# Kernel tuning notes

Hardware: AMD Instinct MI355X
Metric: run time of the kernel (lower is better)

## Reference

```python
import jax, jax.numpy as jnp
import numpy as np

N_MOD, DEPTH, DIM_E = 8, 2, 128   # n experts, routing depth, codebook dim
C, H, W, B = 128, 32, 32, 16      # channels, spatial, batch


def setup_inputs() -> dict:
    key = jax.random.key(0)
    ks = jax.random.split(key, 5)
    s = lambda fan: 1.0 / np.sqrt(fan)
    x = jax.random.normal(ks[0], (B, C, H, W), jnp.float32)
    # controller: 1x1 conv == linear on globally-pooled features
    W_ctl = jax.random.normal(ks[1], (DEPTH * DIM_E, C), jnp.float32) * s(C)
    b_ctl = jnp.zeros((DEPTH * DIM_E,), jnp.float32)
    # VQ codebook: [dim_embeddings, n_modules]
    emb = jax.random.normal(ks[2], (DIM_E, N_MOD), jnp.float32)
    # expert conv weights (shared across depth, as in the module list)
    W_exp = jax.random.normal(ks[3], (N_MOD, C, C, 3, 3), jnp.float32) * s(C * 9)
    b_exp = jnp.zeros((N_MOD, C), jnp.float32)
    return {"x": x, "W_ctl": W_ctl, "b_ctl": b_ctl, "emb": emb,
            "W_exp": W_exp, "b_exp": b_exp}


def reference(x, W_ctl, b_ctl, emb, W_exp, b_exp):
    Bn = x.shape[0]
    # controller: 1x1 conv then AdaptiveAvgPool2d(1) == pool then linear
    pooled = x.mean(axis=(2, 3))                      # [B, C]
    ctl = (pooled @ W_ctl.T + b_ctl).reshape(Bn, DIM_E, DEPTH)  # [B, D, depth]
    # nearest-embedding routing indices (argmin over codebook, no grad path)
    d2 = ((ctl[:, :, :, None] - emb[None, :, None, :]) ** 2).sum(axis=1)  # [B, depth, n_mod]
    idx = jnp.argmin(d2, axis=-1)                     # [B, depth]
    # quantized controller codes from detached ctl (same indices here)
    ctl_sg = jax.lax.stop_gradient(ctl)
    d2n = ((ctl_sg[:, :, :, None] - emb[None, :, None, :]) ** 2).sum(axis=1)
    idx_n = jnp.argmin(d2n, axis=-1)                  # [B, depth]
    ctl_nearest = jnp.transpose(emb[:, idx_n], (1, 0, 2))  # [B, D, depth]
    # dispatch: run all experts as one grouped conv, then gather per example
    Wflat = W_exp.reshape(N_MOD * C, C, 3, 3)
    y = x
    for t in range(DEPTH):
        out = jax.lax.conv_general_dilated(
            y, Wflat, window_strides=(1, 1), padding='SAME',
            dimension_numbers=('NCHW', 'OIHW', 'NCHW'))  # [B, n_mod*C, H, W]
        out = out.reshape(Bn, N_MOD, C, H, W) + b_exp[None, :, :, None, None]
        out = jax.nn.relu(out)
        y = out[jnp.arange(Bn), idx[:, t]]            # [B, C, H, W]
    return y, ctl, ctl_nearest
```

## Files before the change

kernel.cpp:

```cpp
#include <hip/hip_runtime.h>
#include <cstddef>

#define NMOD   8
#define DEPTH_ 2
#define DIME   128
#define CCH    128
#define HH     32
#define WW     32
#define BB     16
#define HWPX   (HH*WW)

#define CO_TILE 4
#define CI_TILE 4
#define CI_HALF 64
#define TROWS   34
#define TSTRIDE 36
#define PF_N    4

__global__ __launch_bounds__(256) void pool_kernel(
    const float* __restrict__ x, float* __restrict__ pooled)
{
    const int ch   = blockIdx.x * 4 + (threadIdx.x >> 6);
    const int lane = threadIdx.x & 63;
    const float* xc = x + (size_t)ch * HWPX;

    float4 s4 = {0.f, 0.f, 0.f, 0.f};
    #pragma unroll
    for (int k = 0; k < 4; ++k) {
        const float4 v = *(const float4*)(xc + (size_t)(lane + k * 64) * 4);
        s4.x += v.x; s4.y += v.y; s4.z += v.z; s4.w += v.w;
    }
    float s = (s4.x + s4.y) + (s4.z + s4.w);
    #pragma unroll
    for (int off = 32; off; off >>= 1) s += __shfl_xor(s, off, 64);
    if (lane == 0) pooled[ch] = s * (1.0f / HWPX);
}

__global__ __launch_bounds__(256) void ctl_kernel(
    const float* __restrict__ pooled, const float* __restrict__ W_ctl,
    const float* __restrict__ b_ctl, const float* __restrict__ emb,
    float* __restrict__ ctl_out, float* __restrict__ ctln_out,
    int* __restrict__ idx_out)
{
    const int b   = blockIdx.x;
    const int tid = threadIdx.x;

    __shared__ float pld[CCH];
    __shared__ float ctlrow[DIME * DEPTH_];
    __shared__ float d2s[DEPTH_ * NMOD];
    __shared__ int   sidx[DEPTH_];

    if (tid < CCH / 4)
        ((float4*)pld)[tid] = ((const float4*)(pooled + (size_t)b * CCH))[tid];
    __syncthreads();

    {
        const float4* wr = (const float4*)(W_ctl + (size_t)tid * CCH);
        const float4* pv = (const float4*)pld;
        float a0 = 0.f, a1 = 0.f, a2 = 0.f, a3 = 0.f;
        #pragma unroll
        for (int k = 0; k < 32; k += 4) {
            const float4 w0 = wr[k + 0], p0 = pv[k + 0];
            const float4 w1 = wr[k + 1], p1 = pv[k + 1];
            const float4 w2 = wr[k + 2], p2 = pv[k + 2];
            const float4 w3 = wr[k + 3], p3 = pv[k + 3];
            a0 = fmaf(w0.x, p0.x, fmaf(w0.y, p0.y, fmaf(w0.z, p0.z, fmaf(w0.w, p0.w, a0))));
            a1 = fmaf(w1.x, p1.x, fmaf(w1.y, p1.y, fmaf(w1.z, p1.z, fmaf(w1.w, p1.w, a1))));
            a2 = fmaf(w2.x, p2.x, fmaf(w2.y, p2.y, fmaf(w2.z, p2.z, fmaf(w2.w, p2.w, a2))));
            a3 = fmaf(w3.x, p3.x, fmaf(w3.y, p3.y, fmaf(w3.z, p3.z, fmaf(w3.w, p3.w, a3))));
        }
        const float s = b_ctl[tid] + ((a0 + a1) + (a2 + a3));
        ctlrow[tid] = s;
        ctl_out[(size_t)b * (DIME * DEPTH_) + tid] = s;
    }
    __syncthreads();

    {
        const int p = tid >> 4;
        const int sub = tid & 15;
        const int t = p >> 3, mm = p & 7;
        float s = 0.f;
        #pragma unroll
        for (int k = 0; k < 8; ++k) {
            const int e = sub * 8 + k;
            const float d = ctlrow[e * DEPTH_ + t] - emb[e * NMOD + mm];
            s = fmaf(d, d, s);
        }
        #pragma unroll
        for (int off = 8; off; off >>= 1) s += __shfl_xor(s, off, 16);
        if (sub == 0) d2s[p] = s;
    }
    __syncthreads();

    if (tid < DEPTH_) {
        float best = d2s[tid * NMOD];
        int bi = 0;
        for (int m = 1; m < NMOD; ++m) {
            const float d = d2s[tid * NMOD + m];
            if (d < best) { best = d; bi = m; }
        }
        sidx[tid] = bi;
        idx_out[b * DEPTH_ + tid] = bi;
    }
    __syncthreads();

    {
        const int e = tid >> 1, t = tid & 1;
        ctln_out[(size_t)b * (DIME * DEPTH_) + e * DEPTH_ + t] =
            emb[e * NMOD + sidx[t]];
    }
}

__global__ __launch_bounds__(256, 4) void conv_kernel(
    const float* __restrict__ in, const float* __restrict__ W_exp,
    const int* __restrict__ idx, int t,
    float* __restrict__ p0, float* __restrict__ p1)
{
    const int cog  = blockIdx.x;
    const int b    = blockIdx.y;
    const int half = blockIdx.z;
    const int tid  = threadIdx.x;
    const int ci_base = half * CI_HALF;
    const int m   = __builtin_amdgcn_readfirstlane(idx[b * DEPTH_ + t]);
    const int co0 = cog * CO_TILE;

    __shared__ float tile[CI_TILE * TROWS * TSTRIDE];

    const float* wb = W_exp + (size_t)m * CCH * (CCH * 9) + (size_t)ci_base * 9;
    const float* wc0 = wb + (size_t)(co0 + 0) * (CCH * 9);
    const float* wc1 = wb + (size_t)(co0 + 1) * (CCH * 9);
    const float* wc2 = wb + (size_t)(co0 + 2) * (CCH * 9);
    const float* wc3 = wb + (size_t)(co0 + 3) * (CCH * 9);

    for (int i = tid; i < CI_TILE * TROWS * TSTRIDE; i += 256) tile[i] = 0.f;

    const int h  = tid >> 3;
    const int w4 = (tid & 7) * 4;

    float acc[4][CO_TILE];
    #pragma unroll
    for (int p = 0; p < 4; ++p)
        #pragma unroll
        for (int c = 0; c < CO_TILE; ++c) acc[p][c] = 0.f;

    const float* ing = in + (size_t)b * CCH * HWPX + (size_t)ci_base * HWPX;

    float4 pf[PF_N];
    #pragma unroll
    for (int k = 0; k < PF_N; ++k)
        pf[k] = *(const float4*)(ing + (size_t)(tid + k * 256) * 4);

    __syncthreads();

    for (int ci0 = 0; ci0 < CI_HALF; ci0 += CI_TILE) {
        #pragma unroll
        for (int k = 0; k < PF_N; ++k) {
            const int q   = tid + k * 256;
            const int cil = q >> 8;
            const int p4  = q & 255;
            const int hh  = p4 >> 3;
            const int ww  = (p4 & 7) * 4;
            float* dst = &tile[cil * (TROWS * TSTRIDE) + (hh + 1) * TSTRIDE + (ww + 1)];
            dst[0] = pf[k].x; dst[1] = pf[k].y; dst[2] = pf[k].z; dst[3] = pf[k].w;
        }
        if (ci0 + CI_TILE < CI_HALF) {
            const float* src = ing + (size_t)(ci0 + CI_TILE) * HWPX;
            #pragma unroll
            for (int k = 0; k < PF_N; ++k)
                pf[k] = *(const float4*)(src + (size_t)(tid + k * 256) * 4);
        }
        __syncthreads();

        #pragma unroll
        for (int cil = 0; cil < CI_TILE; ++cil) {
            const float* trow = &tile[cil * (TROWS * TSTRIDE)];
            const int    cw   = (ci0 + cil) * 9;

            float wr[CO_TILE][9];
            #pragma unroll
            for (int j = 0; j < 9; ++j) {
                wr[0][j] = wc0[cw + j];
                wr[1][j] = wc1[cw + j];
                wr[2][j] = wc2[cw + j];
                wr[3][j] = wc3[cw + j];
            }

            #pragma unroll
            for (int kh = 0; kh < 3; ++kh) {
                const float* r = trow + (h + kh) * TSTRIDE + w4;
                const float4 a4 = *(const float4*)(r);
                const float2 a2 = *(const float2*)(r + 4);
                const float in6[6] = {a4.x, a4.y, a4.z, a4.w, a2.x, a2.y};
                #pragma unroll
                for (int kw = 0; kw < 3; ++kw) {
                    #pragma unroll
                    for (int p = 0; p < 4; ++p) {
                        const float v = in6[p + kw];
                        acc[p][0] = fmaf(v, wr[0][kh * 3 + kw], acc[p][0]);
                        acc[p][1] = fmaf(v, wr[1][kh * 3 + kw], acc[p][1]);
                        acc[p][2] = fmaf(v, wr[2][kh * 3 + kw], acc[p][2]);
                        acc[p][3] = fmaf(v, wr[3][kh * 3 + kw], acc[p][3]);
                    }
                }
            }
        }
        __syncthreads();
    }

    float* outp = (half == 0) ? p0 : p1;
    float* ob = outp + ((size_t)b * CCH + co0) * HWPX + h * WW + w4;
    #pragma unroll
    for (int c = 0; c < CO_TILE; ++c) {
        float4 v;
        v.x = acc[0][c]; v.y = acc[1][c]; v.z = acc[2][c]; v.w = acc[3][c];
        *(float4*)(ob + (size_t)c * HWPX) = v;
    }
}

__global__ __launch_bounds__(256) void combine_kernel(
    const float* __restrict__ p0, const float* __restrict__ p1,
    const float* __restrict__ b_exp, const int* __restrict__ idx, int t,
    float* __restrict__ outp)
{
    const int i4 = blockIdx.x * 256 + threadIdx.x;
    const int b  = i4 >> 15;
    const int co = (i4 >> 8) & (CCH - 1);
    const int m  = idx[b * DEPTH_ + t];
    const float bv = b_exp[m * CCH + co];
    const float4 a = ((const float4*)p0)[i4];
    const float4 c = ((const float4*)p1)[i4];
    float4 v;
    v.x = fmaxf(a.x + c.x + bv, 0.f);
    v.y = fmaxf(a.y + c.y + bv, 0.f);
    v.z = fmaxf(a.z + c.z + bv, 0.f);
    v.w = fmaxf(a.w + c.w + bv, 0.f);
    ((float4*)outp)[i4] = v;
}

extern "C" void kernel_launch(void* const* d_in, const int* in_sizes, int n_in,
                              void* d_out, int out_size, void* d_ws, size_t ws_size,
                              hipStream_t stream) {
    const float* x     = (const float*)d_in[0];
    const float* W_ctl = (const float*)d_in[1];
    const float* b_ctl = (const float*)d_in[2];
    const float* emb   = (const float*)d_in[3];
    const float* W_exp = (const float*)d_in[4];
    const float* b_exp = (const float*)d_in[5];

    float* out      = (float*)d_out;
    float* y_out    = out;
    float* ctl_out  = out + (size_t)BB * CCH * HWPX;
    float* ctln_out = ctl_out + BB * DIME * DEPTH_;

    float* wsA    = (float*)d_ws;
    int*   idxp   = (int*)((char*)d_ws + (size_t)BB * CCH * HWPX * sizeof(float));
    float* pooled = (float*)((char*)idxp + 128);
    float* xbuf   = (float*)d_in[0];

    const int NY4 = (BB * CCH * HWPX) / 4;

    pool_kernel<<<(BB * CCH) / 4, 256, 0, stream>>>(x, pooled);
    ctl_kernel<<<BB, 256, 0, stream>>>(pooled, W_ctl, b_ctl, emb,
                                       ctl_out, ctln_out, idxp);

    conv_kernel<<<dim3(CCH / CO_TILE, BB, 2), 256, 0, stream>>>(
        x, W_exp, idxp, 0, y_out, wsA);
    combine_kernel<<<NY4 / 256, 256, 0, stream>>>(
        y_out, wsA, b_exp, idxp, 0, wsA);

    conv_kernel<<<dim3(CCH / CO_TILE, BB, 2), 256, 0, stream>>>(
        wsA, W_exp, idxp, 1, y_out, xbuf);
    combine_kernel<<<NY4 / 256, 256, 0, stream>>>(
        y_out, xbuf, b_exp, idxp, 1, y_out);
}
```

Measured before the change: 220.6 us.

## Replace LDS-tiled conv input staging with direct global loads and zero-page halo

The conv kernel no longer stages input channels through a shared-memory tile with barriers. Each thread now loads its own 3x3 halo (a float4 plus left and right neighbours for three rows) straight from global memory, one channel ahead in registers. Out-of-bounds positions point at a small zeroed page that the pool kernel writes, with a zero stride. This removes LDS writes and the __syncthreads per channel group, but makes every thread issue many small overlapping global loads that rely on L1/L2 for reuse.

```diff
diff --git a/kernel.cpp b/kernel.cpp
--- a/kernel.cpp
+++ b/kernel.cpp
@@ -11,15 +11,14 @@
 #define HWPX   (HH*WW)
 
 #define CO_TILE 4
-#define CI_TILE 4
 #define CI_HALF 64
-#define TROWS   34
-#define TSTRIDE 36
-#define PF_N    4
 
 __global__ __launch_bounds__(256) void pool_kernel(
-    const float* __restrict__ x, float* __restrict__ pooled)
-{
+    const float* __restrict__ x, float* __restrict__ pooled,
+    float* __restrict__ zpage)
+{
+    if (blockIdx.x == 0 && threadIdx.x < 64) zpage[threadIdx.x] = 0.f;
+
     const int ch   = blockIdx.x * 4 + (threadIdx.x >> 6);
     const int lane = threadIdx.x & 63;
     const float* xc = x + (size_t)ch * HWPX;
@@ -113,7 +112,7 @@
 
 __global__ __launch_bounds__(256, 4) void conv_kernel(
     const float* __restrict__ in, const float* __restrict__ W_exp,
-    const int* __restrict__ idx, int t,
+    const int* __restrict__ idx, int t, const float* __restrict__ zpage,
     float* __restrict__ p0, float* __restrict__ p1)
 {
     const int cog  = blockIdx.x;
@@ -124,18 +123,30 @@
     const int m   = __builtin_amdgcn_readfirstlane(idx[b * DEPTH_ + t]);
     const int co0 = cog * CO_TILE;
 
-    __shared__ float tile[CI_TILE * TROWS * TSTRIDE];
-
     const float* wb = W_exp + (size_t)m * CCH * (CCH * 9) + (size_t)ci_base * 9;
     const float* wc0 = wb + (size_t)(co0 + 0) * (CCH * 9);
     const float* wc1 = wb + (size_t)(co0 + 1) * (CCH * 9);
     const float* wc2 = wb + (size_t)(co0 + 2) * (CCH * 9);
     const float* wc3 = wb + (size_t)(co0 + 3) * (CCH * 9);
 
-    for (int i = tid; i < CI_TILE * TROWS * TSTRIDE; i += 256) tile[i] = 0.f;
-
     const int h  = tid >> 3;
-    const int w4 = (tid & 7) * 4;
+    const int wp = tid & 7;
+    const int w4 = wp * 4;
+
+    const float* xb = in + (size_t)b * CCH * HWPX + (size_t)ci_base * HWPX;
+    const float* pm[3]; const float* pl[3]; const float* pr[3];
+    int sm[3], sl[3], sr[3];
+    #pragma unroll
+    for (int kh = 0; kh < 3; ++kh) {
+        const int row = h + kh - 1;
+        const bool vr = (unsigned)row < 32u;
+        const float* rbase = xb + row * WW;
+        const bool vl = vr && (wp > 0);
+        const bool vR = vr && (wp < 7);
+        pm[kh] = vr ? (rbase + w4)     : zpage;  sm[kh] = vr ? HWPX : 0;
+        pl[kh] = vl ? (rbase + w4 - 1) : zpage;  sl[kh] = vl ? HWPX : 0;
+        pr[kh] = vR ? (rbase + w4 + 4) : zpage;  sr[kh] = vR ? HWPX : 0;
+    }
 
     float acc[4][CO_TILE];
     #pragma unroll
@@ -143,69 +154,58 @@
         #pragma unroll
         for (int c = 0; c < CO_TILE; ++c) acc[p][c] = 0.f;
 
-    const float* ing = in + (size_t)b * CCH * HWPX + (size_t)ci_base * HWPX;
-
-    float4 pf[PF_N];
-    #pragma unroll
-    for (int k = 0; k < PF_N; ++k)
-        pf[k] = *(const float4*)(ing + (size_t)(tid + k * 256) * 4);
-
-    __syncthreads();
-
-    for (int ci0 = 0; ci0 < CI_HALF; ci0 += CI_TILE) {
-        #pragma unroll
-        for (int k = 0; k < PF_N; ++k) {
-            const int q   = tid + k * 256;
-            const int cil = q >> 8;
-            const int p4  = q & 255;
-            const int hh  = p4 >> 3;
-            const int ww  = (p4 & 7) * 4;
-            float* dst = &tile[cil * (TROWS * TSTRIDE) + (hh + 1) * TSTRIDE + (ww + 1)];
-            dst[0] = pf[k].x; dst[1] = pf[k].y; dst[2] = pf[k].z; dst[3] = pf[k].w;
-        }
-        if (ci0 + CI_TILE < CI_HALF) {
-            const float* src = ing + (size_t)(ci0 + CI_TILE) * HWPX;
+    float4 cm[3]; float cl[3], cr[3];
+    #pragma unroll
+    for (int kh = 0; kh < 3; ++kh) {
+        cm[kh] = *(const float4*)pm[kh];
+        cl[kh] = *pl[kh];
+        cr[kh] = *pr[kh];
+    }
+
+    auto body = [&](int ci) {
+        const int cw = ci * 9;
+        float wr[CO_TILE][9];
+        #pragma unroll
+        for (int j = 0; j < 9; ++j) {
+            wr[0][j] = wc0[cw + j];
+            wr[1][j] = wc1[cw + j];
+            wr[2][j] = wc2[cw + j];
+            wr[3][j] = wc3[cw + j];
+        }
+        #pragma unroll
+        for (int kh = 0; kh < 3; ++kh) {
+            const float in6[6] = {cl[kh], cm[kh].x, cm[kh].y, cm[kh].z,
+                                  cm[kh].w, cr[kh]};
             #pragma unroll
-            for (int k = 0; k < PF_N; ++k)
-                pf[k] = *(const float4*)(src + (size_t)(tid + k * 256) * 4);
-        }
-        __syncthreads();
-
-        #pragma unroll
-        for (int cil = 0; cil < CI_TILE; ++cil) {
-            const float* trow = &tile[cil * (TROWS * TSTRIDE)];
-            const int    cw   = (ci0 + cil) * 9;
-
-            float wr[CO_TILE][9];
-            #pragma unroll
-            for (int j = 0; j < 9; ++j) {
-                wr[0][j] = wc0[cw + j];
-                wr[1][j] = wc1[cw + j];
-                wr[2][j] = wc2[cw + j];
-                wr[3][j] = wc3[cw + j];
-            }
-
-            #pragma unroll
-            for (int kh = 0; kh < 3; ++kh) {
-                const float* r = trow + (h + kh) * TSTRIDE + w4;
-                const float4 a4 = *(const float4*)(r);
-                const float2 a2 = *(const float2*)(r + 4);
-                const float in6[6] = {a4.x, a4.y, a4.z, a4.w, a2.x, a2.y};
+            for (int kw = 0; kw < 3; ++kw) {
                 #pragma unroll
-                for (int kw = 0; kw < 3; ++kw) {
-                    #pragma unroll
-                    for (int p = 0; p < 4; ++p) {
-                        const float v = in6[p + kw];
-                        acc[p][0] = fmaf(v, wr[0][kh * 3 + kw], acc[p][0]);
-                        acc[p][1] = fmaf(v, wr[1][kh * 3 + kw], acc[p][1]);
-                        acc[p][2] = fmaf(v, wr[2][kh * 3 + kw], acc[p][2]);
-                        acc[p][3] = fmaf(v, wr[3][kh * 3 + kw], acc[p][3]);
-                    }
+                for (int p = 0; p < 4; ++p) {
+                    const float v = in6[p + kw];
+                    acc[p][0] = fmaf(v, wr[0][kh * 3 + kw], acc[p][0]);
+                    acc[p][1] = fmaf(v, wr[1][kh * 3 + kw], acc[p][1]);
+                    acc[p][2] = fmaf(v, wr[2][kh * 3 + kw], acc[p][2]);
+                    acc[p][3] = fmaf(v, wr[3][kh * 3 + kw], acc[p][3]);
                 }
             }
         }
-        __syncthreads();
-    }
+    };
+
+    for (int ci = 0; ci < CI_HALF - 1; ++ci) {
+        float4 nm[3]; float nl[3], nr[3];
+        #pragma unroll
+        for (int kh = 0; kh < 3; ++kh) {
+            pm[kh] += sm[kh]; pl[kh] += sl[kh]; pr[kh] += sr[kh];
+            nm[kh] = *(const float4*)pm[kh];
+            nl[kh] = *pl[kh];
+            nr[kh] = *pr[kh];
+        }
+        body(ci);
+        #pragma unroll
+        for (int kh = 0; kh < 3; ++kh) {
+            cm[kh] = nm[kh]; cl[kh] = nl[kh]; cr[kh] = nr[kh];
+        }
+    }
+    body(CI_HALF - 1);
 
     float* outp = (half == 0) ? p0 : p1;
     float* ob = outp + ((size_t)b * CCH + co0) * HWPX + h * WW + w4;
@@ -255,21 +255,22 @@
     float* wsA    = (float*)d_ws;
     int*   idxp   = (int*)((char*)d_ws + (size_t)BB * CCH * HWPX * sizeof(float));
     float* pooled = (float*)((char*)idxp + 128);
+    float* zpage  = pooled + BB * CCH;
     float* xbuf   = (float*)d_in[0];
 
     const int NY4 = (BB * CCH * HWPX) / 4;
 
-    pool_kernel<<<(BB * CCH) / 4, 256, 0, stream>>>(x, pooled);
+    pool_kernel<<<(BB * CCH) / 4, 256, 0, stream>>>(x, pooled, zpage);
     ctl_kernel<<<BB, 256, 0, stream>>>(pooled, W_ctl, b_ctl, emb,
                                        ctl_out, ctln_out, idxp);
 
     conv_kernel<<<dim3(CCH / CO_TILE, BB, 2), 256, 0, stream>>>(
-        x, W_exp, idxp, 0, y_out, wsA);
+        x, W_exp, idxp, 0, zpage, y_out, wsA);
     combine_kernel<<<NY4 / 256, 256, 0, stream>>>(
         y_out, wsA, b_exp, idxp, 0, wsA);
 
     conv_kernel<<<dim3(CCH / CO_TILE, BB, 2), 256, 0, stream>>>(
-        wsA, W_exp, idxp, 1, y_out, xbuf);
+        wsA, W_exp, idxp, 1, zpage, y_out, xbuf);
     combine_kernel<<<NY4 / 256, 256, 0, stream>>>(
         y_out, xbuf, b_exp, idxp, 1, y_out);
 }
```

Measured after the change: 355.9 us. +61.3%, slower.
